# Optimization experiments

Measured on AMD Instinct MI355X. Metric: run time of the kernel, lower is better.

Reference implementation:

```python
import jax, jax.numpy as jnp
import numpy as np

N_NODES = 50000
N_EDGES = 600000
N_GRAPHS = 64
D_IN = 128
D_HID = 128
D_LAT = 64
BN_EPS = 1e-5


def setup_inputs() -> dict:
    key = jax.random.key(0)
    ks = jax.random.split(key, 8)
    x = jax.random.normal(ks[0], (N_NODES, D_IN), dtype=jnp.float32)
    edge_index = jax.random.randint(ks[1], (2, N_EDGES), 0, N_NODES, dtype=jnp.int64 if jax.config.jax_enable_x64 else jnp.int32)
    batch = jnp.sort(jax.random.randint(ks[2], (N_NODES,), 0, N_GRAPHS))
    d_cat = 13 * D_IN  # x + (mean,max,min,std) x (identity,amp,att)
    s = 1.0 / np.sqrt(d_cat)
    W0 = jax.random.normal(ks[3], (d_cat, D_HID), dtype=jnp.float32) * s
    W1 = jax.random.normal(ks[4], (13 * D_HID, D_HID), dtype=jnp.float32) * s
    W2 = jax.random.normal(ks[5], (13 * D_HID, D_HID), dtype=jnp.float32) * s
    fcW = jax.random.normal(ks[6], (D_HID, D_LAT), dtype=jnp.float32) * (1.0 / np.sqrt(D_HID))
    return {
        "x": x, "edge_index": edge_index, "batch": batch,
        "W0": W0, "b0": jnp.zeros((D_HID,), jnp.float32),
        "W1": W1, "b1": jnp.zeros((D_HID,), jnp.float32),
        "W2": W2, "b2": jnp.zeros((D_HID,), jnp.float32),
        "bn_gamma": jnp.ones((D_HID,), jnp.float32),
        "bn_beta": jnp.zeros((D_HID,), jnp.float32),
        "fcW": fcW, "fcb": jnp.zeros((D_LAT,), jnp.float32),
    }


def _pna_conv(h, W, b, src, dst, deg, delta):
    # h: [N, d]; messages gathered from source nodes per edge: [E, d]
    m = h[src]
    cnt = jnp.maximum(deg, 1.0)[:, None]
    ssum = jax.ops.segment_sum(m, dst, num_segments=N_NODES)
    mean = ssum / cnt
    ssq = jax.ops.segment_sum(m * m, dst, num_segments=N_NODES)
    std = jnp.sqrt(jnp.maximum(ssq / cnt - mean * mean, 0.0) + 1e-5)
    mx = jax.ops.segment_max(m, dst, num_segments=N_NODES)
    mn = jax.ops.segment_min(m, dst, num_segments=N_NODES)
    has = (deg > 0)[:, None]
    mx = jnp.where(has, mx, 0.0)
    mn = jnp.where(has, mn, 0.0)
    agg = jnp.concatenate([mean, mx, mn, std], axis=-1)  # [N, 4d]
    logd = jnp.log(deg + 1.0)[:, None]
    amp = logd / delta
    att = delta / jnp.maximum(logd, 1e-5)
    feat = jnp.concatenate([h, agg, agg * amp, agg * att], axis=-1)  # [N, 13d]
    return feat @ W + b


def reference(x, edge_index, batch, W0, b0, W1, b1, W2, b2, bn_gamma, bn_beta, fcW, fcb):
    src, dst = edge_index[0], edge_index[1]
    deg = jax.ops.segment_sum(jnp.ones((src.shape[0],), x.dtype), dst, num_segments=N_NODES)
    delta = jnp.mean(jnp.log(deg + 1.0))  # avg log-degree normalizer
    h = jax.nn.relu(_pna_conv(x, W0, b0, src, dst, deg, delta))
    h = jax.nn.relu(_pna_conv(h, W1, b1, src, dst, deg, delta))
    h = jax.nn.relu(_pna_conv(h, W2, b2, src, dst, deg, delta))
    # dropout is identity in eval mode
    pooled = jax.ops.segment_sum(h, batch, num_segments=N_GRAPHS)  # global_add_pool
    mu = jnp.mean(pooled, axis=0)
    var = jnp.var(pooled, axis=0)
    bn = (pooled - mu) / jnp.sqrt(var + BN_EPS) * bn_gamma + bn_beta
    return bn @ fcW + fcb
```

## Files before the change

kernel.cpp:

```cpp
#include <hip/hip_runtime.h>
#include <cstdint>
#include <cstddef>

#define N_NODESC 50000
#define N_PAD    50048
#define N_EDGESC 600000
#define N_GRAPHSC 64
#define D_HIDC   128
#define D_LATC   64
#define D_G      640
#define D_WROW   1664

typedef unsigned short u16;
typedef unsigned int   u32;

typedef _Float16 f16x8 __attribute__((ext_vector_type(8)));
typedef _Float16 f16x2 __attribute__((ext_vector_type(2)));
typedef float    f32x4 __attribute__((ext_vector_type(4)));
typedef float    f32x2 __attribute__((ext_vector_type(2)));

__device__ __forceinline__ u16 f2h(float f) {
    return __builtin_bit_cast(u16, (_Float16)f);
}
__device__ __forceinline__ float h2f(u16 u) {
    return (float)__builtin_bit_cast(_Float16, u);
}

__device__ __forceinline__ void gll16(void* lds, const void* g) {
    __builtin_amdgcn_global_load_lds(
        (const __attribute__((address_space(1))) void*)g,
        (__attribute__((address_space(3))) void*)lds, 16, 0, 0);
}

__global__ void __launch_bounds__(256) k_setup(
        const float* __restrict__ x, const float* __restrict__ W0,
        const float* __restrict__ W1, const float* __restrict__ W2,
        const int* __restrict__ batch,
        u16* __restrict__ h, u16* __restrict__ Wt,
        int* __restrict__ zero_base, int nz, int ZB, int* __restrict__ goff) {
    int b = blockIdx.x;
    int t = threadIdx.x;
    if (b < ZB) {
        int i = b * 256 + t;
        if (i < nz) zero_base[i] = 0;
        return;
    }
    b -= ZB;
    if (b < 12500) {
        int i = b * 256 + t;
        float2 v = ((const float2*)x)[i];
        ((u32*)h)[i] = (u32)f2h(v.x) | ((u32)f2h(v.y) << 16);
        return;
    }
    b -= 12500;
    if (b < 2496) {
        int which = b / 832;
        int i = (b % 832) * 256 + t;
        const float* W = (which == 0) ? W0 : (which == 1) ? W1 : W2;
        int k = i / D_HIDC, j = i % D_HIDC;
        Wt[(size_t)which * D_WROW * D_HIDC + (size_t)j * D_WROW + k] = f2h(W[i]);
        return;
    }
    int g = t;
    if (g <= N_GRAPHSC) {
        int lo = 0, hi = N_NODESC;
        while (lo < hi) {
            int mid = (lo + hi) >> 1;
            if (batch[mid] < g) lo = mid + 1; else hi = mid;
        }
        goff[g] = lo;
    }
}

__global__ void k_count(const int* __restrict__ dst, int* __restrict__ deg) {
    int e = blockIdx.x * 256 + threadIdx.x;
    if (e < N_EDGESC) atomicAdd(&deg[dst[e]], 1);
}

__global__ void __launch_bounds__(256) k_scan_part(
        const int* __restrict__ deg, int* __restrict__ bsum,
        float* __restrict__ lsum) {
    __shared__ int s[256];
    __shared__ float ls[256];
    int idx = blockIdx.x * 256 + threadIdx.x;
    int v = (idx < N_NODESC) ? deg[idx] : 0;
    s[threadIdx.x] = v;
    ls[threadIdx.x] = (idx < N_NODESC) ? logf((float)v + 1.0f) : 0.0f;
    __syncthreads();
    for (int o = 128; o > 0; o >>= 1) {
        if (threadIdx.x < o) {
            s[threadIdx.x] += s[threadIdx.x + o];
            ls[threadIdx.x] += ls[threadIdx.x + o];
        }
        __syncthreads();
    }
    if (threadIdx.x == 0) { bsum[blockIdx.x] = s[0]; lsum[blockIdx.x] = ls[0]; }
}

__global__ void __launch_bounds__(256) k_scan_block(
        int* __restrict__ bsum, const float* __restrict__ lsum,
        float* __restrict__ delta_p) {
    __shared__ int s[256];
    __shared__ float ls[256];
    int t = threadIdx.x;
    int v = (t < 196) ? bsum[t] : 0;
    s[t] = v;
    ls[t] = (t < 196) ? lsum[t] : 0.0f;
    __syncthreads();
    for (int o = 1; o < 256; o <<= 1) {
        int add = (t >= o) ? s[t - o] : 0;
        __syncthreads();
        s[t] += add;
        __syncthreads();
    }
    if (t < 196) bsum[t] = s[t] - v;
    for (int o = 128; o > 0; o >>= 1) {
        if (t < o) ls[t] += ls[t + o];
        __syncthreads();
    }
    if (t == 0) delta_p[0] = ls[0] * (1.0f / (float)N_NODESC);
}

__global__ void __launch_bounds__(256) k_scan_final(
        const int* __restrict__ deg, const int* __restrict__ bsum,
        int* __restrict__ row_off) {
    __shared__ int s[256];
    int t = threadIdx.x;
    int idx = blockIdx.x * 256 + t;
    int v = (idx < N_NODESC) ? deg[idx] : 0;
    s[t] = v; __syncthreads();
    for (int o = 1; o < 256; o <<= 1) {
        int add = (t >= o) ? s[t - o] : 0;
        __syncthreads();
        s[t] += add;
        __syncthreads();
    }
    int excl = s[t] - v + bsum[blockIdx.x];
    if (idx < N_NODESC) row_off[idx] = excl;
    if (idx == 0) row_off[N_NODESC] = N_EDGESC;
}

__global__ void k_fill_csr(const int* __restrict__ src, const int* __restrict__ dst,
                           const int* __restrict__ row_off, int* __restrict__ cursor,
                           int* __restrict__ csr_src) {
    int e = blockIdx.x * 256 + threadIdx.x;
    if (e < N_EDGESC) {
        int d = dst[e];
        int pos = row_off[d] + atomicAdd(&cursor[d], 1);
        csr_src[pos] = src[e];
    }
}


__global__ void __launch_bounds__(256) k_aggregate(
        const u16* __restrict__ h, const int* __restrict__ row_off,
        const int* __restrict__ csr_src, u16* __restrict__ G) {
    int n = blockIdx.x * 4 + (threadIdx.x >> 6);
    if (n >= N_NODESC) return;
    int lane = threadIdx.x & 63;
    int half = lane >> 5, l32 = lane & 31;
    int c4 = 4 * l32;
    int beg = row_off[n], end = row_off[n + 1];
    f32x2 s01 = {0.f, 0.f}, s23 = {0.f, 0.f};
    f32x2 q01 = {0.f, 0.f}, q23 = {0.f, 0.f};
    const _Float16 NEG = (_Float16)(-65504.0f), POS = (_Float16)(65504.0f);
    f16x2 mx01 = {NEG, NEG}, mx23 = {NEG, NEG};
    f16x2 mn01 = {POS, POS}, mn23 = {POS, POS};

    #define PROC(u) { \
        f16x2 p01 = __builtin_bit_cast(f16x2, (u).x); \
        f16x2 p23 = __builtin_bit_cast(f16x2, (u).y); \
        f32x2 c01 = __builtin_convertvector(p01, f32x2); \
        f32x2 c23 = __builtin_convertvector(p23, f32x2); \
        s01 += c01; s23 += c23; \
        q01 += c01 * c01; q23 += c23 * c23; \
        mx01 = __builtin_elementwise_max(mx01, p01); \
        mx23 = __builtin_elementwise_max(mx23, p23); \
        mn01 = __builtin_elementwise_min(mn01, p01); \
        mn23 = __builtin_elementwise_min(mn23, p23); }

    int i = beg + half;
    for (; i + 2 < end; i += 4) {
        int ea = csr_src[i], eb = csr_src[i + 2];
        uint2 ua = *(const uint2*)(h + (size_t)ea * D_HIDC + c4);
        uint2 ub = *(const uint2*)(h + (size_t)eb * D_HIDC + c4);
        PROC(ua);
        PROC(ub);
    }
    if (i < end) {
        int ea = csr_src[i];
        uint2 ua = *(const uint2*)(h + (size_t)ea * D_HIDC + c4);
        PROC(ua);
    }
    #undef PROC

    s01.x += __shfl_xor(s01.x, 32); s01.y += __shfl_xor(s01.y, 32);
    s23.x += __shfl_xor(s23.x, 32); s23.y += __shfl_xor(s23.y, 32);
    q01.x += __shfl_xor(q01.x, 32); q01.y += __shfl_xor(q01.y, 32);
    q23.x += __shfl_xor(q23.x, 32); q23.y += __shfl_xor(q23.y, 32);
    mx01 = __builtin_elementwise_max(mx01,
        __builtin_bit_cast(f16x2, __shfl_xor(__builtin_bit_cast(int, mx01), 32)));
    mx23 = __builtin_elementwise_max(mx23,
        __builtin_bit_cast(f16x2, __shfl_xor(__builtin_bit_cast(int, mx23), 32)));
    mn01 = __builtin_elementwise_min(mn01,
        __builtin_bit_cast(f16x2, __shfl_xor(__builtin_bit_cast(int, mn01), 32)));
    mn23 = __builtin_elementwise_min(mn23,
        __builtin_bit_cast(f16x2, __shfl_xor(__builtin_bit_cast(int, mn23), 32)));

    int d = end - beg;
    float inv = 1.0f / fmaxf((float)d, 1.0f);
    float me0 = s01.x * inv, me1 = s01.y * inv, me2 = s23.x * inv, me3 = s23.y * inv;
    float sd0 = sqrtf(fmaxf(q01.x * inv - me0 * me0, 0.0f) + 1e-5f);
    float sd1 = sqrtf(fmaxf(q01.y * inv - me1 * me1, 0.0f) + 1e-5f);
    float sd2 = sqrtf(fmaxf(q23.x * inv - me2 * me2, 0.0f) + 1e-5f);
    float sd3 = sqrtf(fmaxf(q23.y * inv - me3 * me3, 0.0f) + 1e-5f);
    float fx0 = (float)mx01.x, fx1 = (float)mx01.y;
    float fx2 = (float)mx23.x, fx3 = (float)mx23.y;
    float fn0 = (float)mn01.x, fn1 = (float)mn01.y;
    float fn2 = (float)mn23.x, fn3 = (float)mn23.y;
    if (d == 0) {
        fx0 = fx1 = fx2 = fx3 = 0.0f;
        fn0 = fn1 = fn2 = fn3 = 0.0f;
    }
    u16* base = G + (size_t)n * D_G;
    #define PK2(a, b) ((u32)f2h(a) | ((u32)f2h(b) << 16))
    if (half == 0) {
        *(uint2*)(base + c4) = *(const uint2*)(h + (size_t)n * D_HIDC + c4);
        uint2 m; m.x = PK2(me0, me1); m.y = PK2(me2, me3);
        *(uint2*)(base + 128 + c4) = m;
        uint2 X; X.x = PK2(fx0, fx1); X.y = PK2(fx2, fx3);
        *(uint2*)(base + 256 + c4) = X;
    } else {
        uint2 N_; N_.x = PK2(fn0, fn1); N_.y = PK2(fn2, fn3);
        *(uint2*)(base + 384 + c4) = N_;
        uint2 S; S.x = PK2(sd0, sd1); S.y = PK2(sd2, sd3);
        *(uint2*)(base + 512 + c4) = S;
    }
    #undef PK2
}

__global__ void __launch_bounds__(256) k_gemm(
        const u16* __restrict__ G, const u16* __restrict__ Wt,
        const int* __restrict__ deg, const float* __restrict__ delta_p,
        const float* __restrict__ bias, u16* __restrict__ hout) {
    __shared__ _Float16 A2[128 * 64];
    __shared__ _Float16 A3[128 * 64];
    __shared__ _Float16 Bt[64 * 64];
    const _Float16* Wf = (const _Float16*)Wt;
    const _Float16* Gf = (const _Float16*)G;
    int n0 = blockIdx.x * 64;
    int t = threadIdx.x;
    int w = t >> 6, lane = t & 63;
    int srow8 = lane >> 3, sslot = lane & 7;
    int stg = (sslot ^ srow8) * 8;
    int q4 = lane >> 4, r16 = lane & 15;
    int sx0 = (q4 ^ (lane & 7)) * 8;
    int sx1 = ((q4 + 4) ^ (lane & 7)) * 8;
    int col = lane & 15;

    float delta = delta_p[0];
    float atv[4];
    _Float16 amh[4];
    #pragma unroll
    for (int nt = 0; nt < 4; nt++) {
        int node = n0 + nt * 16 + col;
        float logd = logf((float)deg[node] + 1.0f);
        amh[nt] = (_Float16)(logd / delta);
        atv[nt] = delta / fmaxf(logd, 1e-5f);
    }

    f32x4 acc[2][4], ac3[2][4];
    #pragma unroll
    for (int a = 0; a < 2; a++)
        #pragma unroll
        for (int b = 0; b < 4; b++) {
            acc[a][b] = (f32x4){0.f, 0.f, 0.f, 0.f};
            ac3[a][b] = (f32x4){0.f, 0.f, 0.f, 0.f};
        }

    for (int ki = 0; ki < 8; ki++) {
        int k0 = ki * 64;
        __syncthreads();
        #pragma unroll
        for (int r = 0; r < 4; r++) {
            int arow = (r * 4 + w) * 8 + srow8;
            gll16(&A2[(r * 4 + w) * 512], Wf + (size_t)arow * D_WROW + 640 + k0 + stg);
            gll16(&A3[(r * 4 + w) * 512], Wf + (size_t)arow * D_WROW + 1152 + k0 + stg);
        }
        #pragma unroll
        for (int q = 0; q < 2; q++) {
            int brow = (q * 4 + w) * 8 + srow8;
            gll16(&Bt[(q * 4 + w) * 512], Gf + (size_t)(n0 + brow) * D_G + 128 + k0 + stg);
        }
        __syncthreads();
        f16x8 w2a0 = *(const f16x8*)&A2[(w * 32 + r16) * 64 + sx0];
        f16x8 w2a1 = *(const f16x8*)&A2[(w * 32 + r16) * 64 + sx1];
        f16x8 w2b0 = *(const f16x8*)&A2[(w * 32 + 16 + r16) * 64 + sx0];
        f16x8 w2b1 = *(const f16x8*)&A2[(w * 32 + 16 + r16) * 64 + sx1];
        f16x8 w3a0 = *(const f16x8*)&A3[(w * 32 + r16) * 64 + sx0];
        f16x8 w3a1 = *(const f16x8*)&A3[(w * 32 + r16) * 64 + sx1];
        f16x8 w3b0 = *(const f16x8*)&A3[(w * 32 + 16 + r16) * 64 + sx0];
        f16x8 w3b1 = *(const f16x8*)&A3[(w * 32 + 16 + r16) * 64 + sx1];
        #pragma unroll
        for (int nt = 0; nt < 4; nt++) {
            f16x8 b0 = *(const f16x8*)&Bt[(nt * 16 + r16) * 64 + sx0];
            f16x8 b1 = *(const f16x8*)&Bt[(nt * 16 + r16) * 64 + sx1];
            f16x8 bm0 = b0 * amh[nt];
            f16x8 bm1 = b1 * amh[nt];
            acc[0][nt] = __builtin_amdgcn_mfma_f32_16x16x32_f16(w2a0, bm0, acc[0][nt], 0, 0, 0);
            acc[1][nt] = __builtin_amdgcn_mfma_f32_16x16x32_f16(w2b0, bm0, acc[1][nt], 0, 0, 0);
            acc[0][nt] = __builtin_amdgcn_mfma_f32_16x16x32_f16(w2a1, bm1, acc[0][nt], 0, 0, 0);
            acc[1][nt] = __builtin_amdgcn_mfma_f32_16x16x32_f16(w2b1, bm1, acc[1][nt], 0, 0, 0);
            ac3[0][nt] = __builtin_amdgcn_mfma_f32_16x16x32_f16(w3a0, b0, ac3[0][nt], 0, 0, 0);
            ac3[1][nt] = __builtin_amdgcn_mfma_f32_16x16x32_f16(w3b0, b0, ac3[1][nt], 0, 0, 0);
            ac3[0][nt] = __builtin_amdgcn_mfma_f32_16x16x32_f16(w3a1, b1, ac3[0][nt], 0, 0, 0);
            ac3[1][nt] = __builtin_amdgcn_mfma_f32_16x16x32_f16(w3b1, b1, ac3[1][nt], 0, 0, 0);
        }
    }
    for (int ki = 0; ki < 10; ki++) {
        int k0 = ki * 64;
        __syncthreads();
        #pragma unroll
        for (int r = 0; r < 4; r++) {
            int arow = (r * 4 + w) * 8 + srow8;
            gll16(&A2[(r * 4 + w) * 512], Wf + (size_t)arow * D_WROW + k0 + stg);
        }
        #pragma unroll
        for (int q = 0; q < 2; q++) {
            int brow = (q * 4 + w) * 8 + srow8;
            gll16(&Bt[(q * 4 + w) * 512], Gf + (size_t)(n0 + brow) * D_G + k0 + stg);
        }
        __syncthreads();
        f16x8 a00 = *(const f16x8*)&A2[(w * 32 + r16) * 64 + sx0];
        f16x8 a01 = *(const f16x8*)&A2[(w * 32 + r16) * 64 + sx1];
        f16x8 a10 = *(const f16x8*)&A2[(w * 32 + 16 + r16) * 64 + sx0];
        f16x8 a11 = *(const f16x8*)&A2[(w * 32 + 16 + r16) * 64 + sx1];
        #pragma unroll
        for (int nt = 0; nt < 4; nt++) {
            f16x8 b0 = *(const f16x8*)&Bt[(nt * 16 + r16) * 64 + sx0];
            f16x8 b1 = *(const f16x8*)&Bt[(nt * 16 + r16) * 64 + sx1];
            acc[0][nt] = __builtin_amdgcn_mfma_f32_16x16x32_f16(a00, b0, acc[0][nt], 0, 0, 0);
            acc[1][nt] = __builtin_amdgcn_mfma_f32_16x16x32_f16(a10, b0, acc[1][nt], 0, 0, 0);
            acc[0][nt] = __builtin_amdgcn_mfma_f32_16x16x32_f16(a01, b1, acc[0][nt], 0, 0, 0);
            acc[1][nt] = __builtin_amdgcn_mfma_f32_16x16x32_f16(a11, b1, acc[1][nt], 0, 0, 0);
        }
    }
    int rowq = q4 * 4;
    #pragma unroll
    for (int nt = 0; nt < 4; nt++) {
        int node = n0 + nt * 16 + col;
        float at = atv[nt];
        #pragma unroll
        for (int mt = 0; mt < 2; mt++) {
            int jb = w * 32 + mt * 16 + rowq;
            f32x4 v = acc[mt][nt], v3 = ac3[mt][nt];
            ushort4 o;
            o.x = f2h(fmaxf(v.x + at * v3.x + bias[jb], 0.0f));
            o.y = f2h(fmaxf(v.y + at * v3.y + bias[jb + 1], 0.0f));
            o.z = f2h(fmaxf(v.z + at * v3.z + bias[jb + 2], 0.0f));
            o.w = f2h(fmaxf(v.w + at * v3.w + bias[jb + 3], 0.0f));
            *(ushort4*)&hout[(size_t)node * D_HIDC + jb] = o;
        }
    }
}


__global__ void __launch_bounds__(256) k_pool(
        const u16* __restrict__ h, const int* __restrict__ goff,
        float* __restrict__ pooled) {
    __shared__ float sm[256];
    int g = blockIdx.x >> 2, s = blockIdx.x & 3;
    int gb = goff[g], ge = goff[g + 1];
    int len = ge - gb;
    int q = (len + 3) >> 2;
    int nb = gb + s * q;
    int ne = min(nb + q, ge);
    int t = threadIdx.x;
    int j = t & 127, half = t >> 7;
    float acc = 0.0f;
    for (int n = nb + half; n < ne; n += 2)
        acc += h2f(h[(size_t)n * D_HIDC + j]);
    sm[t] = acc; __syncthreads();
    if (t < 128) {
        float v = sm[t] + sm[t + 128];
        atomicAdd(&pooled[g * D_HIDC + j], v);
    }
}

__global__ void __launch_bounds__(128) k_bn_fc(
        const float* __restrict__ pooled, const float* __restrict__ gamma,
        const float* __restrict__ beta, const float* __restrict__ fcW,
        const float* __restrict__ fcb, float* __restrict__ out) {
    __shared__ float bn[D_HIDC];
    int g = blockIdx.x, t = threadIdx.x;
    float s = 0.f, q = 0.f;
    for (int gg = 0; gg < N_GRAPHSC; gg++) {
        float v = pooled[gg * D_HIDC + t];
        s += v; q += v * v;
    }
    float mu = s * (1.0f / N_GRAPHSC);
    float var = q * (1.0f / N_GRAPHSC) - mu * mu;
    float inv = 1.0f / sqrtf(var + 1e-5f);
    bn[t] = (pooled[g * D_HIDC + t] - mu) * inv * gamma[t] + beta[t];
    __syncthreads();
    if (t < D_LATC) {
        float accum = fcb[t];
        for (int j = 0; j < D_HIDC; j++) accum += bn[j] * fcW[j * D_LATC + t];
        out[g * D_LATC + t] = accum;
    }
}


extern "C" void kernel_launch(void* const* d_in, const int* in_sizes, int n_in,
                              void* d_out, int out_size, void* d_ws, size_t ws_size,
                              hipStream_t stream) {
    const float* x     = (const float*)d_in[0];
    const int*   ei    = (const int*)d_in[1];
    const int*   batch = (const int*)d_in[2];
    const float* W0 = (const float*)d_in[3];
    const float* b0 = (const float*)d_in[4];
    const float* W1 = (const float*)d_in[5];
    const float* b1 = (const float*)d_in[6];
    const float* W2 = (const float*)d_in[7];
    const float* b2 = (const float*)d_in[8];
    const float* gamma = (const float*)d_in[9];
    const float* beta  = (const float*)d_in[10];
    const float* fcW   = (const float*)d_in[11];
    const float* fcb   = (const float*)d_in[12];
    float* out = (float*)d_out;
    const int* srcv = ei;
    const int* dstv = ei + N_EDGESC;

    char* p = (char*)d_ws;
    auto alloc = [&](size_t bytes) -> char* {
        char* r = p;
        p += (bytes + 255) & ~(size_t)255;
        return r;
    };
    int*   deg_cnt = (int*)alloc((size_t)N_PAD * 4);
    int*   cursor  = (int*)alloc((size_t)N_NODESC * 4);
    float* delta_p = (float*)alloc(4);
    float* pooled  = (float*)alloc((size_t)N_GRAPHSC * D_HIDC * 4);
    char*  zero_end = p;
    int*   row_off = (int*)alloc((size_t)(N_NODESC + 1) * 4);
    int*   goff    = (int*)alloc((size_t)(N_GRAPHSC + 1) * 4);
    int*   bsum    = (int*)alloc(256 * 4);
    float* lsum    = (float*)alloc(256 * 4);
    int*   csr_src = (int*)alloc((size_t)N_EDGESC * 4);
    u16*   Wt      = (u16*)alloc((size_t)3 * D_WROW * D_HIDC * 2);
    u16*   hA      = (u16*)alloc((size_t)N_PAD * D_HIDC * 2);
    u16*   hB      = (u16*)alloc((size_t)N_PAD * D_HIDC * 2);
    u16*   G       = (u16*)alloc((size_t)N_PAD * D_G * 2);

    int nz = (int)((zero_end - (char*)deg_cnt) / 4);
    int ZB = (nz + 255) / 256;
    int setup_grid = ZB + 12500 + 2496 + 1;
    k_setup<<<setup_grid, 256, 0, stream>>>(x, W0, W1, W2, batch,
                                            hB, Wt, deg_cnt, nz, ZB, goff);
    k_count<<<(N_EDGESC + 255) / 256, 256, 0, stream>>>(dstv, deg_cnt);
    k_scan_part<<<196, 256, 0, stream>>>(deg_cnt, bsum, lsum);
    k_scan_block<<<1, 256, 0, stream>>>(bsum, lsum, delta_p);
    k_scan_final<<<196, 256, 0, stream>>>(deg_cnt, bsum, row_off);
    k_fill_csr<<<(N_EDGESC + 255) / 256, 256, 0, stream>>>(srcv, dstv, row_off, cursor, csr_src);

    const float* bs[3] = {b0, b1, b2};
    const u16* h_in[3]  = {hB, hA, hB};
    u16*       h_out[3] = {hA, hB, hA};
    size_t wsz = (size_t)D_WROW * D_HIDC;
    for (int l = 0; l < 3; l++) {
        k_aggregate<<<(N_NODESC + 3) / 4, 256, 0, stream>>>(
            h_in[l], row_off, csr_src, G);
        k_gemm<<<N_PAD / 64, 256, 0, stream>>>(
            G, Wt + (size_t)l * wsz, deg_cnt, delta_p, bs[l], h_out[l]);
    }
    k_pool<<<4 * N_GRAPHSC, 256, 0, stream>>>(h_out[2], goff, pooled);
    k_bn_fc<<<N_GRAPHSC, 128, 0, stream>>>(pooled, gamma, beta, fcW, fcb, out);
}
```

Baseline: 450.8 us.

## Merge GEMM K-loops to reuse G tile across three weight segments; unroll aggregation

```diff
diff --git a/kernel.cpp b/kernel.cpp
--- a/kernel.cpp
+++ b/kernel.cpp
@@ -161,9 +161,9 @@
     int half = lane >> 5, l32 = lane & 31;
     int c4 = 4 * l32;
     int beg = row_off[n], end = row_off[n + 1];
+    const _Float16 NEG = (_Float16)(-65504.0f), POS = (_Float16)(65504.0f);
     f32x2 s01 = {0.f, 0.f}, s23 = {0.f, 0.f};
     f32x2 q01 = {0.f, 0.f}, q23 = {0.f, 0.f};
-    const _Float16 NEG = (_Float16)(-65504.0f), POS = (_Float16)(65504.0f);
     f16x2 mx01 = {NEG, NEG}, mx23 = {NEG, NEG};
     f16x2 mn01 = {POS, POS}, mn23 = {POS, POS};
 
@@ -180,17 +180,19 @@
         mn23 = __builtin_elementwise_min(mn23, p23); }
 
     int i = beg + half;
-    for (; i + 2 < end; i += 4) {
-        int ea = csr_src[i], eb = csr_src[i + 2];
-        uint2 ua = *(const uint2*)(h + (size_t)ea * D_HIDC + c4);
-        uint2 ub = *(const uint2*)(h + (size_t)eb * D_HIDC + c4);
-        PROC(ua);
-        PROC(ub);
-    }
-    if (i < end) {
-        int ea = csr_src[i];
-        uint2 ua = *(const uint2*)(h + (size_t)ea * D_HIDC + c4);
-        PROC(ua);
+    for (; i + 6 < end; i += 8) {
+        int e0 = csr_src[i],     e1 = csr_src[i + 2];
+        int e2 = csr_src[i + 4], e3 = csr_src[i + 6];
+        uint2 u0 = *(const uint2*)(h + (size_t)e0 * D_HIDC + c4);
+        uint2 u1 = *(const uint2*)(h + (size_t)e1 * D_HIDC + c4);
+        uint2 u2 = *(const uint2*)(h + (size_t)e2 * D_HIDC + c4);
+        uint2 u3 = *(const uint2*)(h + (size_t)e3 * D_HIDC + c4);
+        PROC(u0); PROC(u1); PROC(u2); PROC(u3);
+    }
+    for (; i < end; i += 2) {
+        int e0 = csr_src[i];
+        uint2 u0 = *(const uint2*)(h + (size_t)e0 * D_HIDC + c4);
+        PROC(u0);
     }
     #undef PROC
 
@@ -198,18 +200,16 @@
     s23.x += __shfl_xor(s23.x, 32); s23.y += __shfl_xor(s23.y, 32);
     q01.x += __shfl_xor(q01.x, 32); q01.y += __shfl_xor(q01.y, 32);
     q23.x += __shfl_xor(q23.x, 32); q23.y += __shfl_xor(q23.y, 32);
-    mx01 = __builtin_elementwise_max(mx01,
-        __builtin_bit_cast(f16x2, __shfl_xor(__builtin_bit_cast(int, mx01), 32)));
-    mx23 = __builtin_elementwise_max(mx23,
-        __builtin_bit_cast(f16x2, __shfl_xor(__builtin_bit_cast(int, mx23), 32)));
-    mn01 = __builtin_elementwise_min(mn01,
-        __builtin_bit_cast(f16x2, __shfl_xor(__builtin_bit_cast(int, mn01), 32)));
-    mn23 = __builtin_elementwise_min(mn23,
-        __builtin_bit_cast(f16x2, __shfl_xor(__builtin_bit_cast(int, mn23), 32)));
+    #define MRG(v, OP) v = OP(v, \
+        __builtin_bit_cast(f16x2, __shfl_xor(__builtin_bit_cast(int, v), 32)))
+    MRG(mx01, __builtin_elementwise_max); MRG(mx23, __builtin_elementwise_max);
+    MRG(mn01, __builtin_elementwise_min); MRG(mn23, __builtin_elementwise_min);
+    #undef MRG
 
     int d = end - beg;
     float inv = 1.0f / fmaxf((float)d, 1.0f);
-    float me0 = s01.x * inv, me1 = s01.y * inv, me2 = s23.x * inv, me3 = s23.y * inv;
+    float me0 = s01.x * inv, me1 = s01.y * inv;
+    float me2 = s23.x * inv, me3 = s23.y * inv;
     float sd0 = sqrtf(fmaxf(q01.x * inv - me0 * me0, 0.0f) + 1e-5f);
     float sd1 = sqrtf(fmaxf(q01.y * inv - me1 * me1, 0.0f) + 1e-5f);
     float sd2 = sqrtf(fmaxf(q23.x * inv - me2 * me2, 0.0f) + 1e-5f);
@@ -243,6 +243,7 @@
         const u16* __restrict__ G, const u16* __restrict__ Wt,
         const int* __restrict__ deg, const float* __restrict__ delta_p,
         const float* __restrict__ bias, u16* __restrict__ hout) {
+    __shared__ _Float16 A1[128 * 64];
     __shared__ _Float16 A2[128 * 64];
     __shared__ _Float16 A3[128 * 64];
     __shared__ _Float16 Bt[64 * 64];
@@ -278,71 +279,73 @@
             ac3[a][b] = (f32x4){0.f, 0.f, 0.f, 0.f};
         }
 
-    for (int ki = 0; ki < 8; ki++) {
+    for (int ki = 0; ki < 10; ki++) {
         int k0 = ki * 64;
+        bool sreg = (k0 >= 128);
         __syncthreads();
         #pragma unroll
         for (int r = 0; r < 4; r++) {
-            int arow = (r * 4 + w) * 8 + srow8;
-            gll16(&A2[(r * 4 + w) * 512], Wf + (size_t)arow * D_WROW + 640 + k0 + stg);
-            gll16(&A3[(r * 4 + w) * 512], Wf + (size_t)arow * D_WROW + 1152 + k0 + stg);
+            int rr = r * 4 + w;
+            const _Float16* wrow = Wf + (size_t)(rr * 8 + srow8) * D_WROW;
+            gll16(&A1[rr * 512], wrow + k0 + stg);
+        }
+        if (sreg) {
+            #pragma unroll
+            for (int r = 0; r < 4; r++) {
+                int rr = r * 4 + w;
+                const _Float16* wrow = Wf + (size_t)(rr * 8 + srow8) * D_WROW;
+                gll16(&A2[rr * 512], wrow + 512 + k0 + stg);
+                gll16(&A3[rr * 512], wrow + 1024 + k0 + stg);
+            }
         }
         #pragma unroll
         for (int q = 0; q < 2; q++) {
-            int brow = (q * 4 + w) * 8 + srow8;
-            gll16(&Bt[(q * 4 + w) * 512], Gf + (size_t)(n0 + brow) * D_G + 128 + k0 + stg);
-        }
-        __syncthreads();
-        f16x8 w2a0 = *(const f16x8*)&A2[(w * 32 + r16) * 64 + sx0];
-        f16x8 w2a1 = *(const f16x8*)&A2[(w * 32 + r16) * 64 + sx1];
-        f16x8 w2b0 = *(const f16x8*)&A2[(w * 32 + 16 + r16) * 64 + sx0];
-        f16x8 w2b1 = *(const f16x8*)&A2[(w * 32 + 16 + r16) * 64 + sx1];
-        f16x8 w3a0 = *(const f16x8*)&A3[(w * 32 + r16) * 64 + sx0];
-        f16x8 w3a1 = *(const f16x8*)&A3[(w * 32 + r16) * 64 + sx1];
-        f16x8 w3b0 = *(const f16x8*)&A3[(w * 32 + 16 + r16) * 64 + sx0];
-        f16x8 w3b1 = *(const f16x8*)&A3[(w * 32 + 16 + r16) * 64 + sx1];
-        #pragma unroll
-        for (int nt = 0; nt < 4; nt++) {
-            f16x8 b0 = *(const f16x8*)&Bt[(nt * 16 + r16) * 64 + sx0];
-            f16x8 b1 = *(const f16x8*)&Bt[(nt * 16 + r16) * 64 + sx1];
-            f16x8 bm0 = b0 * amh[nt];
-            f16x8 bm1 = b1 * amh[nt];
-            acc[0][nt] = __builtin_amdgcn_mfma_f32_16x16x32_f16(w2a0, bm0, acc[0][nt], 0, 0, 0);
-            acc[1][nt] = __builtin_amdgcn_mfma_f32_16x16x32_f16(w2b0, bm0, acc[1][nt], 0, 0, 0);
-            acc[0][nt] = __builtin_amdgcn_mfma_f32_16x16x32_f16(w2a1, bm1, acc[0][nt], 0, 0, 0);
-            acc[1][nt] = __builtin_amdgcn_mfma_f32_16x16x32_f16(w2b1, bm1, acc[1][nt], 0, 0, 0);
-            ac3[0][nt] = __builtin_amdgcn_mfma_f32_16x16x32_f16(w3a0, b0, ac3[0][nt], 0, 0, 0);
-            ac3[1][nt] = __builtin_amdgcn_mfma_f32_16x16x32_f16(w3b0, b0, ac3[1][nt], 0, 0, 0);
-            ac3[0][nt] = __builtin_amdgcn_mfma_f32_16x16x32_f16(w3a1, b1, ac3[0][nt], 0, 0, 0);
-            ac3[1][nt] = __builtin_amdgcn_mfma_f32_16x16x32_f16(w3b1, b1, ac3[1][nt], 0, 0, 0);
-        }
-    }
-    for (int ki = 0; ki < 10; ki++) {
-        int k0 = ki * 64;
-        __syncthreads();
-        #pragma unroll
-        for (int r = 0; r < 4; r++) {
-            int arow = (r * 4 + w) * 8 + srow8;
-            gll16(&A2[(r * 4 + w) * 512], Wf + (size_t)arow * D_WROW + k0 + stg);
-        }
-        #pragma unroll
-        for (int q = 0; q < 2; q++) {
-            int brow = (q * 4 + w) * 8 + srow8;
-            gll16(&Bt[(q * 4 + w) * 512], Gf + (size_t)(n0 + brow) * D_G + k0 + stg);
-        }
-        __syncthreads();
-        f16x8 a00 = *(const f16x8*)&A2[(w * 32 + r16) * 64 + sx0];
-        f16x8 a01 = *(const f16x8*)&A2[(w * 32 + r16) * 64 + sx1];
-        f16x8 a10 = *(const f16x8*)&A2[(w * 32 + 16 + r16) * 64 + sx0];
-        f16x8 a11 = *(const f16x8*)&A2[(w * 32 + 16 + r16) * 64 + sx1];
-        #pragma unroll
-        for (int nt = 0; nt < 4; nt++) {
-            f16x8 b0 = *(const f16x8*)&Bt[(nt * 16 + r16) * 64 + sx0];
-            f16x8 b1 = *(const f16x8*)&Bt[(nt * 16 + r16) * 64 + sx1];
-            acc[0][nt] = __builtin_amdgcn_mfma_f32_16x16x32_f16(a00, b0, acc[0][nt], 0, 0, 0);
-            acc[1][nt] = __builtin_amdgcn_mfma_f32_16x16x32_f16(a10, b0, acc[1][nt], 0, 0, 0);
-            acc[0][nt] = __builtin_amdgcn_mfma_f32_16x16x32_f16(a01, b1, acc[0][nt], 0, 0, 0);
-            acc[1][nt] = __builtin_amdgcn_mfma_f32_16x16x32_f16(a11, b1, acc[1][nt], 0, 0, 0);
+            int rr = q * 4 + w;
+            gll16(&Bt[rr * 512], Gf + (size_t)(n0 + rr * 8 + srow8) * D_G + k0 + stg);
+        }
+        __syncthreads();
+        f16x8 a00 = *(const f16x8*)&A1[(w * 32 + r16) * 64 + sx0];
+        f16x8 a01 = *(const f16x8*)&A1[(w * 32 + r16) * 64 + sx1];
+        f16x8 a10 = *(const f16x8*)&A1[(w * 32 + 16 + r16) * 64 + sx0];
+        f16x8 a11 = *(const f16x8*)&A1[(w * 32 + 16 + r16) * 64 + sx1];
+        if (!sreg) {
+            #pragma unroll
+            for (int nt = 0; nt < 4; nt++) {
+                f16x8 b0 = *(const f16x8*)&Bt[(nt * 16 + r16) * 64 + sx0];
+                f16x8 b1 = *(const f16x8*)&Bt[(nt * 16 + r16) * 64 + sx1];
+                acc[0][nt] = __builtin_amdgcn_mfma_f32_16x16x32_f16(a00, b0, acc[0][nt], 0, 0, 0);
+                acc[1][nt] = __builtin_amdgcn_mfma_f32_16x16x32_f16(a10, b0, acc[1][nt], 0, 0, 0);
+                acc[0][nt] = __builtin_amdgcn_mfma_f32_16x16x32_f16(a01, b1, acc[0][nt], 0, 0, 0);
+                acc[1][nt] = __builtin_amdgcn_mfma_f32_16x16x32_f16(a11, b1, acc[1][nt], 0, 0, 0);
+            }
+        } else {
+            f16x8 w2a0 = *(const f16x8*)&A2[(w * 32 + r16) * 64 + sx0];
+            f16x8 w2a1 = *(const f16x8*)&A2[(w * 32 + r16) * 64 + sx1];
+            f16x8 w2b0 = *(const f16x8*)&A2[(w * 32 + 16 + r16) * 64 + sx0];
+            f16x8 w2b1 = *(const f16x8*)&A2[(w * 32 + 16 + r16) * 64 + sx1];
+            f16x8 w3a0 = *(const f16x8*)&A3[(w * 32 + r16) * 64 + sx0];
+            f16x8 w3a1 = *(const f16x8*)&A3[(w * 32 + r16) * 64 + sx1];
+            f16x8 w3b0 = *(const f16x8*)&A3[(w * 32 + 16 + r16) * 64 + sx0];
+            f16x8 w3b1 = *(const f16x8*)&A3[(w * 32 + 16 + r16) * 64 + sx1];
+            #pragma unroll
+            for (int nt = 0; nt < 4; nt++) {
+                f16x8 b0 = *(const f16x8*)&Bt[(nt * 16 + r16) * 64 + sx0];
+                f16x8 b1 = *(const f16x8*)&Bt[(nt * 16 + r16) * 64 + sx1];
+                f16x8 bm0 = b0 * amh[nt];
+                f16x8 bm1 = b1 * amh[nt];
+                acc[0][nt] = __builtin_amdgcn_mfma_f32_16x16x32_f16(a00, b0, acc[0][nt], 0, 0, 0);
+                acc[1][nt] = __builtin_amdgcn_mfma_f32_16x16x32_f16(a10, b0, acc[1][nt], 0, 0, 0);
+                acc[0][nt] = __builtin_amdgcn_mfma_f32_16x16x32_f16(a01, b1, acc[0][nt], 0, 0, 0);
+                acc[1][nt] = __builtin_amdgcn_mfma_f32_16x16x32_f16(a11, b1, acc[1][nt], 0, 0, 0);
+                acc[0][nt] = __builtin_amdgcn_mfma_f32_16x16x32_f16(w2a0, bm0, acc[0][nt], 0, 0, 0);
+                acc[1][nt] = __builtin_amdgcn_mfma_f32_16x16x32_f16(w2b0, bm0, acc[1][nt], 0, 0, 0);
+                acc[0][nt] = __builtin_amdgcn_mfma_f32_16x16x32_f16(w2a1, bm1, acc[0][nt], 0, 0, 0);
+                acc[1][nt] = __builtin_amdgcn_mfma_f32_16x16x32_f16(w2b1, bm1, acc[1][nt], 0, 0, 0);
+                ac3[0][nt] = __builtin_amdgcn_mfma_f32_16x16x32_f16(w3a0, b0, ac3[0][nt], 0, 0, 0);
+                ac3[1][nt] = __builtin_amdgcn_mfma_f32_16x16x32_f16(w3b0, b0, ac3[1][nt], 0, 0, 0);
+                ac3[0][nt] = __builtin_amdgcn_mfma_f32_16x16x32_f16(w3a1, b1, ac3[0][nt], 0, 0, 0);
+                ac3[1][nt] = __builtin_amdgcn_mfma_f32_16x16x32_f16(w3b1, b1, ac3[1][nt], 0, 0, 0);
+            }
         }
     }
     int rowq = q4 * 4;
```

After: 425.1 us (median of 2 runs). 5.7% less time.
